# Kernel tuning notes

Hardware: AMD Instinct MI355X
Metric: run time of the kernel (lower is better)

The kernel has to match this reference:

```python
import jax, jax.numpy as jnp
import numpy as np
from jax import lax

N_EXPERTS = 16
TOP_K = 2
D_MODEL = 512
D_FF = 2048


def setup_inputs() -> dict:
    key = jax.random.key(0)
    ks = jax.random.split(key, 7)
    s_in = 1.0 / np.sqrt(D_MODEL)
    s_ff = 1.0 / np.sqrt(D_FF)
    x = jax.random.normal(ks[0], (2, 2048, D_MODEL), dtype=jnp.float32)
    router_w = jax.random.uniform(ks[1], (N_EXPERTS, D_MODEL), jnp.float32, -s_in, s_in)
    router_b = jax.random.uniform(ks[2], (N_EXPERTS,), jnp.float32, -s_in, s_in)
    w1 = jax.random.uniform(ks[3], (N_EXPERTS, D_FF, D_MODEL), jnp.float32, -s_in, s_in)
    b1 = jax.random.uniform(ks[4], (N_EXPERTS, D_FF), jnp.float32, -s_in, s_in)
    w2 = jax.random.uniform(ks[5], (N_EXPERTS, D_MODEL, D_FF), jnp.float32, -s_ff, s_ff)
    b2 = jax.random.uniform(ks[6], (N_EXPERTS, D_MODEL), jnp.float32, -s_ff, s_ff)
    return {"x": x, "router_w": router_w, "router_b": router_b,
            "w1": w1, "b1": b1, "w2": w2, "b2": b2}


def reference(x, router_w, router_b, w1, b1, w2, b2):
    B, S, D = x.shape
    xt = x.reshape(-1, D)                                   # [T, D]
    logits = xt @ router_w.T + router_b                     # [T, E]
    probs = jax.nn.softmax(logits, axis=-1)
    topk_p, topk_i = lax.top_k(probs, TOP_K)                # [T, K]
    # Dense gate matrix: gate[t, e] = topk prob if expert e selected else 0.
    # Weighting by gate reproduces the masked gather/scatter-add exactly.
    onehot = jax.nn.one_hot(topk_i, N_EXPERTS, dtype=probs.dtype)  # [T, K, E]
    gates = jnp.sum(onehot * topk_p[..., None], axis=1)     # [T, E]

    def expert_step(acc, packed):
        w1e, b1e, w2e, b2e, ge = packed                     # per-expert params + gate col [T]
        h = jax.nn.gelu(xt @ w1e.T + b1e, approximate=False)  # [T, D_FF]
        y = h @ w2e.T + b2e                                 # [T, D]
        return acc + y * ge[:, None], None

    out, _ = lax.scan(expert_step, jnp.zeros_like(xt),
                      (w1, b1, w2, b2, gates.T))
    return out.reshape(B, S, D)
```

## Files before the change

kernel.cpp:

```cpp
#include <hip/hip_runtime.h>
#include <stdint.h>

#define T_TOK 4096
#define DM    512
#define DFF   2048
#define NE    16
#define NSLOT (T_TOK * 2)

typedef __attribute__((ext_vector_type(8))) short  bf16x8;
typedef __attribute__((ext_vector_type(4))) float  f32x4;
typedef __attribute__((ext_vector_type(4))) unsigned short us4;
typedef __attribute__((ext_vector_type(8))) unsigned short us8;

static __device__ __forceinline__ unsigned short f2bf(float f) {
    unsigned int u = __float_as_uint(f);
    u += 0x7FFFu + ((u >> 16) & 1u);
    return (unsigned short)(u >> 16);
}

__global__ __launch_bounds__(256) void router_kernel(
    const float* __restrict__ x, const float* __restrict__ rw,
    const float* __restrict__ rb, int* __restrict__ tok_e,
    float* __restrict__ tok_g)
{
    __shared__ float rws[NE * DM];
    int tid = threadIdx.x;
    for (int i = 0; i < 8; ++i) {
        int idx = (tid + i * 256) * 4;
        *(f32x4*)&rws[idx] = *(const f32x4*)&rw[idx];
    }
    __syncthreads();

    int wid = tid >> 6, lane = tid & 63;
    int t = blockIdx.x * 4 + wid;

    float xv[8];
    const float* xp = x + (size_t)t * DM + lane * 8;
    *(f32x4*)&xv[0] = *(const f32x4*)xp;
    *(f32x4*)&xv[4] = *(const f32x4*)(xp + 4);

    float acc[NE];
    for (int e = 0; e < NE; ++e) {
        const float* wp = &rws[e * DM + lane * 8];
        float a = 0.f;
        for (int i = 0; i < 8; ++i) a += xv[i] * wp[i];
        acc[e] = a;
    }
    for (int e = 0; e < NE; ++e) {
        float v = acc[e];
        for (int off = 32; off > 0; off >>= 1) v += __shfl_xor(v, off);
        acc[e] = v + rb[e];
    }
    float m = acc[0];
    for (int e = 1; e < NE; ++e) m = fmaxf(m, acc[e]);
    float p[NE]; float s = 0.f;
    for (int e = 0; e < NE; ++e) { p[e] = expf(acc[e] - m); s += p[e]; }
    float inv = 1.f / s;
    int i0 = 0; float p0 = p[0];
    for (int e = 1; e < NE; ++e) if (p[e] > p0) { p0 = p[e]; i0 = e; }
    int i1 = (i0 == 0) ? 1 : 0; float p1 = p[i1];
    for (int e = 0; e < NE; ++e)
        if (e != i0 && p[e] > p1) { p1 = p[e]; i1 = e; }
    if (lane == 0) {
        tok_e[t * 2]     = i0;  tok_e[t * 2 + 1] = i1;
        tok_g[t * 2]     = p0 * inv;
        tok_g[t * 2 + 1] = p1 * inv;
    }
}

__global__ __launch_bounds__(256) void compact_kernel(
    const int* __restrict__ tok_e, const float* __restrict__ tok_g,
    int* __restrict__ slot_token, float* __restrict__ slot_gate,
    int* __restrict__ eoff )
{
    __shared__ int cnt[NE], cur[NE], offs[NE];
    int tid = threadIdx.x;
    if (tid < NE) cnt[tid] = 0;
    __syncthreads();
    for (int t = tid; t < T_TOK; t += 256) {
        atomicAdd(&cnt[tok_e[t * 2]], 1);
        atomicAdd(&cnt[tok_e[t * 2 + 1]], 1);
    }
    __syncthreads();
    if (tid == 0) {
        int r = 0;
        for (int e = 0; e < NE; ++e) { offs[e] = r; cur[e] = r; r += cnt[e]; }
    }
    __syncthreads();
    if (tid < NE) { eoff[tid] = offs[tid]; eoff[NE + tid] = cnt[tid]; }
    for (int t = tid; t < T_TOK; t += 256) {
        for (int k = 0; k < 2; ++k) {
            int e = tok_e[t * 2 + k];
            int s = atomicAdd(&cur[e], 1);
            slot_token[s] = t;
            slot_gate[s]  = tok_g[t * 2 + k];
        }
    }
}

__global__ __launch_bounds__(256) void gemm1_kernel(
    const float* __restrict__ x, const float* __restrict__ w1,
    const float* __restrict__ b1, const int* __restrict__ slot_token,
    const int* __restrict__ eoff, unsigned short* __restrict__ h)
{
    __shared__ unsigned short smem[18432];
    __shared__ int tokrow[128];
    unsigned short* As = smem;
    unsigned short* Bs = smem + 9216;

    int e   = blockIdx.z;
    int off = eoff[e], cnt = eoff[NE + e];
    int mt  = blockIdx.y;
    if (mt * 128 >= cnt) return;
    int nB    = blockIdx.x * 128;
    int slot0 = off + mt * 128;
    int valid = cnt - mt * 128; if (valid > 128) valid = 128;

    int tid = threadIdx.x;
    if (tid < 128) {
        int s = slot0 + tid; if (s > NSLOT - 1) s = NSLOT - 1;
        tokrow[tid] = (tid < valid) ? slot_token[s] : 0;
    }
    __syncthreads();

    f32x4 acc[16];
    for (int i = 0; i < 16; ++i) acc[i] = (f32x4){0.f, 0.f, 0.f, 0.f};

    const float* wbase = w1 + ((size_t)e * DFF + nB) * DM;
    int wid = tid >> 6, lane = tid & 63;
    int wm = (wid & 1) * 64, wn = (wid >> 1) * 64;
    int q = lane >> 4, c = lane & 15;

    for (int kt = 0; kt < DM / 64; ++kt) {
        for (int i = 0; i < 8; ++i) {
            int u = tid + i * 256;
            int row = u >> 4, c4 = u & 15;
            f32x4 v = *(const f32x4*)(x + (size_t)tokrow[row] * DM + kt * 64 + c4 * 4);
            us4 a; a.x = f2bf(v.x); a.y = f2bf(v.y); a.z = f2bf(v.z); a.w = f2bf(v.w);
            *(us4*)&As[row * 72 + c4 * 4] = a;
            f32x4 w = *(const f32x4*)(wbase + (size_t)row * DM + kt * 64 + c4 * 4);
            us4 b; b.x = f2bf(w.x); b.y = f2bf(w.y); b.z = f2bf(w.z); b.w = f2bf(w.w);
            *(us4*)&Bs[row * 72 + c4 * 4] = b;
        }
        __syncthreads();
        for (int ks = 0; ks < 2; ++ks) {
            bf16x8 af[4], bfv[4];
            for (int i = 0; i < 4; ++i)
                af[i] = *(bf16x8*)&As[(wm + i * 16 + c) * 72 + ks * 32 + q * 8];
            for (int j = 0; j < 4; ++j)
                bfv[j] = *(bf16x8*)&Bs[(wn + j * 16 + c) * 72 + ks * 32 + q * 8];
            for (int i = 0; i < 4; ++i)
                for (int j = 0; j < 4; ++j)
                    acc[i * 4 + j] = __builtin_amdgcn_mfma_f32_16x16x32_bf16(
                        af[i], bfv[j], acc[i * 4 + j], 0, 0, 0);
        }
        __syncthreads();
    }

    unsigned short* bounce = smem;
    for (int i = 0; i < 4; ++i)
        for (int j = 0; j < 4; ++j) {
            int n = nB + wn + j * 16 + c;
            float bias = b1[e * DFF + n];
            f32x4 a = acc[i * 4 + j];
            for (int r = 0; r < 4; ++r) {
                int rowl = wm + i * 16 + q * 4 + r;
                float z = a[r] + bias;
                float g = 0.5f * z * (1.f + erff(z * 0.70710678118654752f));
                bounce[rowl * 136 + wn + j * 16 + c] = f2bf(g);
            }
        }
    __syncthreads();
    for (int i = 0; i < 8; ++i) {
        int row = (tid >> 4) + i * 16;
        if (row < valid) {
            us8 v = *(us8*)&bounce[row * 136 + (tid & 15) * 8];
            *(us8*)&h[(size_t)(slot0 + row) * DFF + nB + (tid & 15) * 8] = v;
        }
    }
}

__global__ __launch_bounds__(256) void gemm2_kernel(
    const unsigned short* __restrict__ h, const float* __restrict__ w2,
    const float* __restrict__ b2, const int* __restrict__ slot_token,
    const float* __restrict__ slot_gate, const int* __restrict__ eoff,
    float* __restrict__ out)
{
    __shared__ unsigned short smem[18432];
    __shared__ int   tokrow[128];
    __shared__ float grow[128];
    unsigned short* As = smem;
    unsigned short* Bs = smem + 9216;

    int e   = blockIdx.z;
    int off = eoff[e], cnt = eoff[NE + e];
    int mt  = blockIdx.y;
    if (mt * 128 >= cnt) return;
    int nB    = blockIdx.x * 128;
    int slot0 = off + mt * 128;
    int valid = cnt - mt * 128; if (valid > 128) valid = 128;

    int tid = threadIdx.x;
    if (tid < 128) {
        int s = slot0 + tid; if (s > NSLOT - 1) s = NSLOT - 1;
        tokrow[tid] = slot_token[s];
        grow[tid]   = slot_gate[s];
    }
    __syncthreads();

    f32x4 acc[16];
    for (int i = 0; i < 16; ++i) acc[i] = (f32x4){0.f, 0.f, 0.f, 0.f};

    const float* wbase = w2 + ((size_t)e * DM + nB) * DFF;
    int wid = tid >> 6, lane = tid & 63;
    int wm = (wid & 1) * 64, wn = (wid >> 1) * 64;
    int q = lane >> 4, c = lane & 15;

    for (int kt = 0; kt < DFF / 64; ++kt) {
        for (int i = 0; i < 4; ++i) {
            int u = tid + i * 256;
            int row = u >> 3, c8 = u & 7;
            int s = slot0 + row; if (s > NSLOT - 1) s = NSLOT - 1;
            us8 v = *(const us8*)&h[(size_t)s * DFF + kt * 64 + c8 * 8];
            *(us8*)&As[row * 72 + c8 * 8] = v;
        }
        for (int i = 0; i < 8; ++i) {
            int u = tid + i * 256;
            int row = u >> 4, c4 = u & 15;
            f32x4 w = *(const f32x4*)(wbase + (size_t)row * DFF + kt * 64 + c4 * 4);
            us4 b; b.x = f2bf(w.x); b.y = f2bf(w.y); b.z = f2bf(w.z); b.w = f2bf(w.w);
            *(us4*)&Bs[row * 72 + c4 * 4] = b;
        }
        __syncthreads();
        for (int ks = 0; ks < 2; ++ks) {
            bf16x8 af[4], bfv[4];
            for (int i = 0; i < 4; ++i)
                af[i] = *(bf16x8*)&As[(wm + i * 16 + c) * 72 + ks * 32 + q * 8];
            for (int j = 0; j < 4; ++j)
                bfv[j] = *(bf16x8*)&Bs[(wn + j * 16 + c) * 72 + ks * 32 + q * 8];
            for (int i = 0; i < 4; ++i)
                for (int j = 0; j < 4; ++j)
                    acc[i * 4 + j] = __builtin_amdgcn_mfma_f32_16x16x32_bf16(
                        af[i], bfv[j], acc[i * 4 + j], 0, 0, 0);
        }
        __syncthreads();
    }

    for (int i = 0; i < 4; ++i)
        for (int j = 0; j < 4; ++j) {
            int n = nB + wn + j * 16 + c;
            float bias = b2[e * DM + n];
            for (int r = 0; r < 4; ++r) {
                int rowl = wm + i * 16 + q * 4 + r;
                if (rowl < valid) {
                    float y = acc[i * 4 + j][r] + bias;
                    atomicAdd(&out[(size_t)tokrow[rowl] * DM + n], grow[rowl] * y);
                }
            }
        }
}

extern "C" void kernel_launch(void* const* d_in, const int* in_sizes, int n_in,
                              void* d_out, int out_size, void* d_ws, size_t ws_size,
                              hipStream_t stream) {
    const float* x  = (const float*)d_in[0];
    const float* rw = (const float*)d_in[1];
    const float* rb = (const float*)d_in[2];
    const float* w1 = (const float*)d_in[3];
    const float* b1 = (const float*)d_in[4];
    const float* w2 = (const float*)d_in[5];
    const float* b2 = (const float*)d_in[6];
    float* out = (float*)d_out;

    char* ws = (char*)d_ws;
    unsigned short* h = (unsigned short*)ws;
    size_t o = (size_t)NSLOT * DFF * 2;
    int*   tok_e      = (int*)(ws + o);   o += (size_t)NSLOT * 4;
    float* tok_g      = (float*)(ws + o); o += (size_t)NSLOT * 4;
    int*   slot_token = (int*)(ws + o);   o += (size_t)NSLOT * 4;
    float* slot_gate  = (float*)(ws + o); o += (size_t)NSLOT * 4;
    int*   eoff       = (int*)(ws + o);

    hipMemsetAsync(d_out, 0, (size_t)T_TOK * DM * 4, stream);
    router_kernel<<<T_TOK / 4, 256, 0, stream>>>(x, rw, rb, tok_e, tok_g);
    compact_kernel<<<1, 256, 0, stream>>>(tok_e, tok_g, slot_token, slot_gate, eoff);
    gemm1_kernel<<<dim3(DFF / 128, 32, NE), 256, 0, stream>>>(
        x, w1, b1, slot_token, eoff, h);
    gemm2_kernel<<<dim3(DM / 128, 32, NE), 256, 0, stream>>>(
        h, w2, b2, slot_token, slot_gate, eoff, out);
}
```

Measured before the change: 324.7 us.

## Preconvert weights to bf16 and use direct global-to-LDS loads with swizzle

```diff
diff --git a/kernel.cpp b/kernel.cpp
--- a/kernel.cpp
+++ b/kernel.cpp
@@ -6,16 +6,44 @@
 #define DFF   2048
 #define NE    16
 #define NSLOT (T_TOK * 2)
+#define NW    (NE * DFF * DM)
 
 typedef __attribute__((ext_vector_type(8))) short  bf16x8;
 typedef __attribute__((ext_vector_type(4))) float  f32x4;
-typedef __attribute__((ext_vector_type(4))) unsigned short us4;
 typedef __attribute__((ext_vector_type(8))) unsigned short us8;
 
 static __device__ __forceinline__ unsigned short f2bf(float f) {
     unsigned int u = __float_as_uint(f);
     u += 0x7FFFu + ((u >> 16) & 1u);
     return (unsigned short)(u >> 16);
+}
+
+static __device__ __forceinline__ void gload_lds16(const void* g, void* l) {
+    __builtin_amdgcn_global_load_lds(
+        (const __attribute__((address_space(1))) void*)g,
+        (__attribute__((address_space(3))) void*)l, 16, 0, 0);
+}
+
+__global__ __launch_bounds__(256) void convert_kernel(
+    const float* __restrict__ w1, const float* __restrict__ w2,
+    const float* __restrict__ x, unsigned short* __restrict__ w1b,
+    unsigned short* __restrict__ w2b, unsigned short* __restrict__ xb)
+{
+    size_t i = ((size_t)blockIdx.x * 256 + threadIdx.x) * 8;
+    const float* src; unsigned short* dst;
+    if (i < (size_t)NW)            { src = w1 + i;      dst = w1b + i; }
+    else if (i < 2 * (size_t)NW)   { src = w2 + (i - NW); dst = w2b + (i - NW); }
+    else {
+        size_t o = i - 2 * (size_t)NW;
+        if (o >= (size_t)T_TOK * DM) return;
+        src = x + o; dst = xb + o;
+    }
+    f32x4 a = *(const f32x4*)src;
+    f32x4 b = *(const f32x4*)(src + 4);
+    us8 v;
+    v[0] = f2bf(a.x); v[1] = f2bf(a.y); v[2] = f2bf(a.z); v[3] = f2bf(a.w);
+    v[4] = f2bf(b.x); v[5] = f2bf(b.y); v[6] = f2bf(b.z); v[7] = f2bf(b.w);
+    *(us8*)dst = v;
 }
 
 __global__ __launch_bounds__(256) void router_kernel(
@@ -71,7 +99,7 @@
 __global__ __launch_bounds__(256) void compact_kernel(
     const int* __restrict__ tok_e, const float* __restrict__ tok_g,
     int* __restrict__ slot_token, float* __restrict__ slot_gate,
-    int* __restrict__ eoff )
+    int* __restrict__ eoff)
 {
     __shared__ int cnt[NE], cur[NE], offs[NE];
     int tid = threadIdx.x;
@@ -99,14 +127,14 @@
 }
 
 __global__ __launch_bounds__(256) void gemm1_kernel(
-    const float* __restrict__ x, const float* __restrict__ w1,
+    const unsigned short* __restrict__ xb, const unsigned short* __restrict__ w1b,
     const float* __restrict__ b1, const int* __restrict__ slot_token,
     const int* __restrict__ eoff, unsigned short* __restrict__ h)
 {
-    __shared__ unsigned short smem[18432];
+    __shared__ unsigned short smem[16384];
     __shared__ int tokrow[128];
     unsigned short* As = smem;
-    unsigned short* Bs = smem + 9216;
+    unsigned short* Bs = smem + 8192;
 
     int e   = blockIdx.z;
     int off = eoff[e], cnt = eoff[NE + e];
@@ -119,84 +147,91 @@
     int tid = threadIdx.x;
     if (tid < 128) {
         int s = slot0 + tid; if (s > NSLOT - 1) s = NSLOT - 1;
-        tokrow[tid] = (tid < valid) ? slot_token[s] : 0;
+        tokrow[tid] = slot_token[s];
     }
     __syncthreads();
 
     f32x4 acc[16];
     for (int i = 0; i < 16; ++i) acc[i] = (f32x4){0.f, 0.f, 0.f, 0.f};
 
-    const float* wbase = w1 + ((size_t)e * DFF + nB) * DM;
-    int wid = tid >> 6, lane = tid & 63;
+    const unsigned short* wb = w1b + ((size_t)e * DFF + nB) * DM;
+    int wid = tid >> 6, l = tid & 63;
     int wm = (wid & 1) * 64, wn = (wid >> 1) * 64;
-    int q = lane >> 4, c = lane & 15;
+    int q = l >> 4, c = l & 15;
 
     for (int kt = 0; kt < DM / 64; ++kt) {
-        for (int i = 0; i < 8; ++i) {
-            int u = tid + i * 256;
-            int row = u >> 4, c4 = u & 15;
-            f32x4 v = *(const f32x4*)(x + (size_t)tokrow[row] * DM + kt * 64 + c4 * 4);
-            us4 a; a.x = f2bf(v.x); a.y = f2bf(v.y); a.z = f2bf(v.z); a.w = f2bf(v.w);
-            *(us4*)&As[row * 72 + c4 * 4] = a;
-            f32x4 w = *(const f32x4*)(wbase + (size_t)row * DM + kt * 64 + c4 * 4);
-            us4 b; b.x = f2bf(w.x); b.y = f2bf(w.y); b.z = f2bf(w.z); b.w = f2bf(w.w);
-            *(us4*)&Bs[row * 72 + c4 * 4] = b;
+        for (int j = 0; j < 4; ++j) {
+            int u = (wid * 4 + j) * 64 + l;
+            int row = u >> 3, sc = (u & 7) ^ (row & 7);
+            gload_lds16(xb + (size_t)tokrow[row] * DM + kt * 64 + sc * 8, &As[u * 8]);
+        }
+        for (int j = 0; j < 4; ++j) {
+            int u = (wid * 4 + j) * 64 + l;
+            int row = u >> 3, sc = (u & 7) ^ (row & 7);
+            gload_lds16(wb + (size_t)row * DM + kt * 64 + sc * 8, &Bs[u * 8]);
         }
         __syncthreads();
         for (int ks = 0; ks < 2; ++ks) {
-            bf16x8 af[4], bfv[4];
-            for (int i = 0; i < 4; ++i)
-                af[i] = *(bf16x8*)&As[(wm + i * 16 + c) * 72 + ks * 32 + q * 8];
-            for (int j = 0; j < 4; ++j)
-                bfv[j] = *(bf16x8*)&Bs[(wn + j * 16 + c) * 72 + ks * 32 + q * 8];
+            int sw = ((ks * 4 + q) ^ (c & 7)) * 8;
+            bf16x8 af[4], bv[4];
+            for (int i = 0; i < 4; ++i) af[i] = *(bf16x8*)&As[(wm + i * 16 + c) * 64 + sw];
+            for (int j = 0; j < 4; ++j) bv[j] = *(bf16x8*)&Bs[(wn + j * 16 + c) * 64 + sw];
             for (int i = 0; i < 4; ++i)
                 for (int j = 0; j < 4; ++j)
                     acc[i * 4 + j] = __builtin_amdgcn_mfma_f32_16x16x32_bf16(
-                        af[i], bfv[j], acc[i * 4 + j], 0, 0, 0);
-        }
-        __syncthreads();
-    }
-
+                        af[i], bv[j], acc[i * 4 + j], 0, 0, 0);
+        }
+        __syncthreads();
+    }
+
+    float bias[4];
+    for (int j = 0; j < 4; ++j) bias[j] = b1[e * DFF + nB + wn + j * 16 + c];
     unsigned short* bounce = smem;
-    for (int i = 0; i < 4; ++i)
-        for (int j = 0; j < 4; ++j) {
-            int n = nB + wn + j * 16 + c;
-            float bias = b1[e * DFF + n];
-            f32x4 a = acc[i * 4 + j];
-            for (int r = 0; r < 4; ++r) {
-                int rowl = wm + i * 16 + q * 4 + r;
-                float z = a[r] + bias;
-                float g = 0.5f * z * (1.f + erff(z * 0.70710678118654752f));
-                bounce[rowl * 136 + wn + j * 16 + c] = f2bf(g);
-            }
-        }
-    __syncthreads();
-    for (int i = 0; i < 8; ++i) {
-        int row = (tid >> 4) + i * 16;
-        if (row < valid) {
-            us8 v = *(us8*)&bounce[row * 136 + (tid & 15) * 8];
-            *(us8*)&h[(size_t)(slot0 + row) * DFF + nB + (tid & 15) * 8] = v;
+    for (int ph = 0; ph < 2; ++ph) {
+        __syncthreads();
+        if ((wid & 1) == ph) {
+            for (int i = 0; i < 4; ++i)
+                for (int j = 0; j < 4; ++j) {
+                    f32x4 a = acc[i * 4 + j];
+                    for (int r = 0; r < 4; ++r) {
+                        int rl = i * 16 + q * 4 + r;
+                        float z = a[r] + bias[j];
+                        float g = 0.5f * z * (1.f + erff(z * 0.70710678118654752f));
+                        bounce[rl * 136 + wn + j * 16 + c] = f2bf(g);
+                    }
+                }
+        }
+        __syncthreads();
+        for (int it = 0; it < 4; ++it) {
+            int u2 = it * 256 + tid;
+            int row = u2 >> 4, ch = u2 & 15;
+            int gr = ph * 64 + row;
+            if (gr < valid)
+                *(us8*)&h[(size_t)(slot0 + gr) * DFF + nB + ch * 8] =
+                    *(us8*)&bounce[row * 136 + ch * 8];
         }
     }
 }
 
 __global__ __launch_bounds__(256) void gemm2_kernel(
-    const unsigned short* __restrict__ h, const float* __restrict__ w2,
+    const unsigned short* __restrict__ h, const unsigned short* __restrict__ w2b,
     const float* __restrict__ b2, const int* __restrict__ slot_token,
     const float* __restrict__ slot_gate, const int* __restrict__ eoff,
     float* __restrict__ out)
 {
-    __shared__ unsigned short smem[18432];
+    __shared__ unsigned short smem[16384];
     __shared__ int   tokrow[128];
     __shared__ float grow[128];
     unsigned short* As = smem;
-    unsigned short* Bs = smem + 9216;
+    unsigned short* Bs = smem + 8192;
 
     int e   = blockIdx.z;
     int off = eoff[e], cnt = eoff[NE + e];
     int mt  = blockIdx.y;
     if (mt * 128 >= cnt) return;
-    int nB    = blockIdx.x * 128;
+    int nB   = (blockIdx.x & 3) * 128;
+    int half = blockIdx.x >> 2;
+    int k0   = half * (DFF / 2);
     int slot0 = off + mt * 128;
     int valid = cnt - mt * 128; if (valid > 128) valid = 128;
 
@@ -211,37 +246,33 @@
     f32x4 acc[16];
     for (int i = 0; i < 16; ++i) acc[i] = (f32x4){0.f, 0.f, 0.f, 0.f};
 
-    const float* wbase = w2 + ((size_t)e * DM + nB) * DFF;
-    int wid = tid >> 6, lane = tid & 63;
+    const unsigned short* wb = w2b + ((size_t)e * DM + nB) * DFF;
+    int wid = tid >> 6, l = tid & 63;
     int wm = (wid & 1) * 64, wn = (wid >> 1) * 64;
-    int q = lane >> 4, c = lane & 15;
-
-    for (int kt = 0; kt < DFF / 64; ++kt) {
-        for (int i = 0; i < 4; ++i) {
-            int u = tid + i * 256;
-            int row = u >> 3, c8 = u & 7;
-            int s = slot0 + row; if (s > NSLOT - 1) s = NSLOT - 1;
-            us8 v = *(const us8*)&h[(size_t)s * DFF + kt * 64 + c8 * 8];
-            *(us8*)&As[row * 72 + c8 * 8] = v;
-        }
-        for (int i = 0; i < 8; ++i) {
-            int u = tid + i * 256;
-            int row = u >> 4, c4 = u & 15;
-            f32x4 w = *(const f32x4*)(wbase + (size_t)row * DFF + kt * 64 + c4 * 4);
-            us4 b; b.x = f2bf(w.x); b.y = f2bf(w.y); b.z = f2bf(w.z); b.w = f2bf(w.w);
-            *(us4*)&Bs[row * 72 + c4 * 4] = b;
+    int q = l >> 4, c = l & 15;
+
+    for (int kt = 0; kt < (DFF / 2) / 64; ++kt) {
+        for (int j = 0; j < 4; ++j) {
+            int u = (wid * 4 + j) * 64 + l;
+            int row = u >> 3, sc = (u & 7) ^ (row & 7);
+            size_t s = slot0 + row; if (s > NSLOT - 1) s = NSLOT - 1;
+            gload_lds16(h + s * DFF + k0 + kt * 64 + sc * 8, &As[u * 8]);
+        }
+        for (int j = 0; j < 4; ++j) {
+            int u = (wid * 4 + j) * 64 + l;
+            int row = u >> 3, sc = (u & 7) ^ (row & 7);
+            gload_lds16(wb + (size_t)row * DFF + k0 + kt * 64 + sc * 8, &Bs[u * 8]);
         }
         __syncthreads();
         for (int ks = 0; ks < 2; ++ks) {
-            bf16x8 af[4], bfv[4];
-            for (int i = 0; i < 4; ++i)
-                af[i] = *(bf16x8*)&As[(wm + i * 16 + c) * 72 + ks * 32 + q * 8];
-            for (int j = 0; j < 4; ++j)
-                bfv[j] = *(bf16x8*)&Bs[(wn + j * 16 + c) * 72 + ks * 32 + q * 8];
+            int sw = ((ks * 4 + q) ^ (c & 7)) * 8;
+            bf16x8 af[4], bv[4];
+            for (int i = 0; i < 4; ++i) af[i] = *(bf16x8*)&As[(wm + i * 16 + c) * 64 + sw];
+            for (int j = 0; j < 4; ++j) bv[j] = *(bf16x8*)&Bs[(wn + j * 16 + c) * 64 + sw];
             for (int i = 0; i < 4; ++i)
                 for (int j = 0; j < 4; ++j)
                     acc[i * 4 + j] = __builtin_amdgcn_mfma_f32_16x16x32_bf16(
-                        af[i], bfv[j], acc[i * 4 + j], 0, 0, 0);
+                        af[i], bv[j], acc[i * 4 + j], 0, 0, 0);
         }
         __syncthreads();
     }
@@ -249,12 +280,12 @@
     for (int i = 0; i < 4; ++i)
         for (int j = 0; j < 4; ++j) {
             int n = nB + wn + j * 16 + c;
-            float bias = b2[e * DM + n];
+            float bias = (half == 0) ? b2[e * DM + n] : 0.f;
             for (int r = 0; r < 4; ++r) {
-                int rowl = wm + i * 16 + q * 4 + r;
-                if (rowl < valid) {
+                int rl = wm + i * 16 + q * 4 + r;
+                if (rl < valid) {
                     float y = acc[i * 4 + j][r] + bias;
-                    atomicAdd(&out[(size_t)tokrow[rowl] * DM + n], grow[rowl] * y);
+                    atomicAdd(&out[(size_t)tokrow[rl] * DM + n], grow[rl] * y);
                 }
             }
         }
@@ -273,8 +304,11 @@
     float* out = (float*)d_out;
 
     char* ws = (char*)d_ws;
-    unsigned short* h = (unsigned short*)ws;
-    size_t o = (size_t)NSLOT * DFF * 2;
+    size_t o = 0;
+    unsigned short* h   = (unsigned short*)(ws + o); o += (size_t)NSLOT * DFF * 2;
+    unsigned short* w1b = (unsigned short*)(ws + o); o += (size_t)NW * 2;
+    unsigned short* w2b = (unsigned short*)(ws + o); o += (size_t)NW * 2;
+    unsigned short* xb  = (unsigned short*)(ws + o); o += (size_t)T_TOK * DM * 2;
     int*   tok_e      = (int*)(ws + o);   o += (size_t)NSLOT * 4;
     float* tok_g      = (float*)(ws + o); o += (size_t)NSLOT * 4;
     int*   slot_token = (int*)(ws + o);   o += (size_t)NSLOT * 4;
@@ -282,10 +316,12 @@
     int*   eoff       = (int*)(ws + o);
 
     hipMemsetAsync(d_out, 0, (size_t)T_TOK * DM * 4, stream);
+    int conv_blocks = (2 * NW + T_TOK * DM) / 8 / 256;
+    convert_kernel<<<conv_blocks, 256, 0, stream>>>(w1, w2, x, w1b, w2b, xb);
     router_kernel<<<T_TOK / 4, 256, 0, stream>>>(x, rw, rb, tok_e, tok_g);
     compact_kernel<<<1, 256, 0, stream>>>(tok_e, tok_g, slot_token, slot_gate, eoff);
-    gemm1_kernel<<<dim3(DFF / 128, 32, NE), 256, 0, stream>>>(
-        x, w1, b1, slot_token, eoff, h);
-    gemm2_kernel<<<dim3(DM / 128, 32, NE), 256, 0, stream>>>(
-        h, w2, b2, slot_token, slot_gate, eoff, out);
-}
+    gemm1_kernel<<<dim3(DFF / 128, 64, NE), 256, 0, stream>>>(
+        xb, w1b, b1, slot_token, eoff, h);
+    gemm2_kernel<<<dim3(8, 64, NE), 256, 0, stream>>>(
+        h, w2b, b2, slot_token, slot_gate, eoff, out);
+}
```

Result: slower. 364.2 us (+12.2%).
